# Kernel tuning notes

Measured on AMD Instinct MI355X. Metric: run time of the kernel, lower is better.

Reference implementation:

```python
import jax, jax.numpy as jnp
import numpy as np

E = 1024
H = 16
DH = E // H
S = 2048
K_NEIGHBOURS = 64
MASKING_VALUE = -1e10  # fp32 branch of the original module


def setup_inputs() -> dict:
    key = jax.random.key(0)
    ks = jax.random.split(key, 5)
    return {
        "x": jax.random.normal(ks[0], (S, E), dtype=jnp.float32),
        "W_qkv": jax.random.normal(ks[1], (3 * E, E), dtype=jnp.float32) * (E ** -0.5),
        "b_qkv": jax.random.normal(ks[2], (3 * E,), dtype=jnp.float32) * 0.02,
        "W_out": jax.random.normal(ks[3], (E, E), dtype=jnp.float32) * (E ** -0.5),
        "b_out": jax.random.normal(ks[4], (E,), dtype=jnp.float32) * 0.02,
    }


def _heads(t):
    # 's (h d) -> h s d'
    return t.reshape(S, H, DH).transpose(1, 0, 2)


def reference(x, W_qkv, b_qkv, W_out, b_out):
    scale = DH ** -0.5
    qkv = x @ W_qkv.T + b_qkv                      # [S, 3E]
    q, k, v = jnp.split(qkv, 3, axis=-1)
    q, k, v = _heads(q), _heads(k), _heads(v)      # [H, S, DH]
    scores = jnp.einsum('hsd,htd->hst', q, k) * scale  # [H, S, S]
    # banded mask: keep |i-j| <= K_NEIGHBOURS
    idx = jnp.arange(S)
    band = jnp.abs(idx[:, None] - idx[None, :]) <= K_NEIGHBOURS  # [S, S]
    scores = jnp.where(band[None, :, :], scores, MASKING_VALUE)
    attn = jax.nn.softmax(scores, axis=-1)
    out = jnp.einsum('hst,htd->hsd', attn, v)      # [H, S, DH]
    out = out.transpose(1, 0, 2).reshape(S, E)      # 'h s d -> s (h d)'
    out = out @ W_out.T + b_out
    return (out, scores)
```

## Files before the change

### kernel.cpp

```cpp
#include <hip/hip_runtime.h>

typedef unsigned short u16;
typedef __attribute__((ext_vector_type(8))) short short8;
typedef __attribute__((ext_vector_type(4))) short short4v;
typedef __attribute__((ext_vector_type(4))) float f32x4;

#define S_LEN 2048
#define EMB   1024
#define NH    16
#define NEGM  (-1e10f)

__device__ __forceinline__ u16 f2bf(float f) {
  unsigned u = __float_as_uint(f);
  u += 0x7fffu + ((u >> 16) & 1u);
  return (u16)(u >> 16);
}

__device__ __forceinline__ void async16(const u16* g, u16* l) {
  __builtin_amdgcn_global_load_lds(
      (const __attribute__((address_space(1))) unsigned int*)g,
      (__attribute__((address_space(3))) unsigned int*)l, 16, 0, 0);
}

__global__ __launch_bounds__(256) void cast3_kernel(
    const float* __restrict__ a, u16* __restrict__ oa, int na,
    const float* __restrict__ b, u16* __restrict__ ob, int nb,
    const float* __restrict__ c, u16* __restrict__ oc, int nc) {
  int t = (blockIdx.x * 256 + threadIdx.x) * 8;
  const float* in;
  u16* out;
  if (t < na) { in = a + t; out = oa + t; }
  else if (t < na + nb) { in = b + (t - na); out = ob + (t - na); }
  else if (t < na + nb + nc) { in = c + (t - na - nb); out = oc + (t - na - nb); }
  else return;
  f32x4 lo = *(const f32x4*)(in);
  f32x4 hi = *(const f32x4*)(in + 4);
  u16 r[8];
  r[0] = f2bf(lo.x); r[1] = f2bf(lo.y); r[2] = f2bf(lo.z); r[3] = f2bf(lo.w);
  r[4] = f2bf(hi.x); r[5] = f2bf(hi.y); r[6] = f2bf(hi.z); r[7] = f2bf(hi.w);
  *(short8*)(out) = *(short8*)r;
}

template <int BM, int BN, int OUT_BF16, int MINW>
__global__ __launch_bounds__(256, MINW) void gemm_kernel(
    const u16* __restrict__ A, const u16* __restrict__ B,
    const float* __restrict__ bias, void* __restrict__ Cout,
    int M, int N, int K, int grid_x, int gemm_blocks,
    float* __restrict__ fill_ptr, long long fill_f4, int fill_blocks) {
  __shared__ u16 As[BM * 64];
  __shared__ u16 Bs[BN * 64];
  const int b = blockIdx.x;
  const int tid = threadIdx.x;

  if (b >= gemm_blocks) {
    const long long fb = b - gemm_blocks;
    f32x4 neg = {NEGM, NEGM, NEGM, NEGM};
    f32x4* p = (f32x4*)fill_ptr;
    const long long stride = (long long)fill_blocks * 256;
    for (long long idx = fb * 256 + tid; idx < fill_f4; idx += stride)
      __builtin_nontemporal_store(neg, p + idx);
    return;
  }

  const int lane = tid & 63, wave = tid >> 6;
  const int lr = lane & 15, lg = lane >> 4;
  const int bx = b % grid_x, by = b / grid_x;
  const int m0 = by * BM, n0 = bx * BN;
  const int wm = (wave >> 1) * (BM / 2), wn = (wave & 1) * (BN / 2);
  constexpr int MI = BM / 32, NJ = BN / 32;

  f32x4 acc[MI][NJ];
#pragma unroll
  for (int i = 0; i < MI; ++i)
#pragma unroll
    for (int j = 0; j < NJ; ++j) acc[i][j] = (f32x4){0.f, 0.f, 0.f, 0.f};

  for (int kt = 0; kt < K; kt += 64) {
#pragma unroll
    for (int it = 0; it < BM / 32; ++it) {
      int f = it * 256 + tid;
      int row = f >> 3, ch = f & 7;
      int sch = ch ^ (row & 7);
      async16(A + (size_t)(m0 + row) * K + kt + sch * 8,
              &As[(it * 256 + wave * 64) * 8]);
    }
#pragma unroll
    for (int it = 0; it < BN / 32; ++it) {
      int f = it * 256 + tid;
      int row = f >> 3, ch = f & 7;
      int sch = ch ^ (row & 7);
      async16(B + (size_t)(n0 + row) * K + kt + sch * 8,
              &Bs[(it * 256 + wave * 64) * 8]);
    }
    __syncthreads();
#pragma unroll
    for (int kk = 0; kk < 2; ++kk) {
      short8 af[MI], bfr[NJ];
      int ca = kk * 4 + lg;
#pragma unroll
      for (int t = 0; t < MI; ++t) {
        int ra = wm + t * 16 + lr;
        af[t] = *(const short8*)&As[ra * 64 + ((ca ^ (ra & 7)) << 3)];
      }
#pragma unroll
      for (int t = 0; t < NJ; ++t) {
        int rb = wn + t * 16 + lr;
        bfr[t] = *(const short8*)&Bs[rb * 64 + ((ca ^ (rb & 7)) << 3)];
      }
#pragma unroll
      for (int i = 0; i < MI; ++i)
#pragma unroll
        for (int j = 0; j < NJ; ++j)
          acc[i][j] = __builtin_amdgcn_mfma_f32_16x16x32_bf16(af[i], bfr[j],
                                                              acc[i][j], 0, 0, 0);
    }
    __syncthreads();
  }
#pragma unroll
  for (int j = 0; j < NJ; ++j) {
    int col = n0 + wn + j * 16 + lr;
    float bv = bias[col];
#pragma unroll
    for (int i = 0; i < MI; ++i) {
#pragma unroll
      for (int r = 0; r < 4; ++r) {
        int row = m0 + wm + i * 16 + lg * 4 + r;
        float v = acc[i][j][r] + bv;
        if (OUT_BF16)
          ((u16*)Cout)[(size_t)row * N + col] = f2bf(v);
        else
          ((float*)Cout)[(size_t)row * N + col] = v;
      }
    }
  }
}

__global__ __launch_bounds__(256, 2) void attn_kernel(
    const u16* __restrict__ qkv,
    float* __restrict__ scores,
    u16* __restrict__ ctx) {
  const int h = blockIdx.y;
  const int i0 = blockIdx.x * 64;
  const int j0 = i0 - 64;
  const int tid = threadIdx.x;
  const int lane = tid & 63, wave = tid >> 6;
  const int lr = lane & 15, lg = lane >> 4;

  __shared__ u16 Kl[192 * 72];
  __shared__ u16 Vt[64 * 200];
  __shared__ u16 Pl[64 * 200];

#pragma unroll
  for (int it = 0; it < 6; ++it) {
    int f = it * 256 + tid;
    int jr = f >> 3, ch = f & 7;
    int j = j0 + jr;
    short8 kv = {0, 0, 0, 0, 0, 0, 0, 0};
    short8 vv = {0, 0, 0, 0, 0, 0, 0, 0};
    if ((unsigned)j < 2048u) {
      kv = *(const short8*)(qkv + (size_t)j * 3072 + 1024 + h * 64 + ch * 8);
      vv = *(const short8*)(qkv + (size_t)j * 3072 + 2048 + h * 64 + ch * 8);
    }
    *(short4v*)&Kl[jr * 72 + ch * 8] = __builtin_shufflevector(kv, kv, 0, 1, 2, 3);
    *(short4v*)&Kl[jr * 72 + ch * 8 + 4] = __builtin_shufflevector(kv, kv, 4, 5, 6, 7);
#pragma unroll
    for (int e = 0; e < 8; ++e) Vt[(ch * 8 + e) * 200 + jr] = (u16)(short)vv[e];
  }
  __syncthreads();

  short8 qf[2];
#pragma unroll
  for (int kk = 0; kk < 2; ++kk)
    qf[kk] = *(const short8*)(qkv + (size_t)(i0 + wave * 16 + lr) * 3072 +
                              h * 64 + kk * 32 + lg * 8);

  f32x4 sa[12];
#pragma unroll
  for (int n = 0; n < 12; ++n) sa[n] = (f32x4){0.f, 0.f, 0.f, 0.f};
#pragma unroll
  for (int kk = 0; kk < 2; ++kk) {
    short8 a = qf[kk];
#pragma unroll
    for (int nt = 0; nt < 12; ++nt) {
      int jr = nt * 16 + lr;
      int d = kk * 32 + lg * 8;
      short4v lo = *(const short4v*)&Kl[jr * 72 + d];
      short4v hi = *(const short4v*)&Kl[jr * 72 + d + 4];
      short8 b = __builtin_shufflevector(lo, hi, 0, 1, 2, 3, 4, 5, 6, 7);
      sa[nt] = __builtin_amdgcn_mfma_f32_16x16x32_bf16(a, b, sa[nt], 0, 0, 0);
    }
  }

  const float scale = 0.125f;
#pragma unroll
  for (int nt = 0; nt < 12; ++nt) {
    int j = j0 + nt * 16 + lr;
#pragma unroll
    for (int r = 0; r < 4; ++r) {
      int i = i0 + wave * 16 + lg * 4 + r;
      bool inb = (j >= i - 64) && (j <= i + 64);
      sa[nt][r] = inb ? sa[nt][r] * scale : NEGM;
    }
  }

  float* srow_base = scores + (size_t)h * 2048 * 2048;
#pragma unroll
  for (int r = 0; r < 4; ++r) {
    int i = i0 + wave * 16 + lg * 4 + r;
    float* rowp = srow_base + (size_t)i * 2048;
#pragma unroll
    for (int nt = 0; nt < 12; ++nt) {
      int j = j0 + nt * 16 + lr;
      if ((unsigned)j < 2048u) rowp[j] = sa[nt][r];
    }
  }

#pragma unroll
  for (int r = 0; r < 4; ++r) {
    float m = sa[0][r];
#pragma unroll
    for (int nt = 1; nt < 12; ++nt) m = fmaxf(m, sa[nt][r]);
#pragma unroll
    for (int off = 1; off < 16; off <<= 1) m = fmaxf(m, __shfl_xor(m, off));
    float p[12], s = 0.f;
#pragma unroll
    for (int nt = 0; nt < 12; ++nt) {
      p[nt] = __expf(sa[nt][r] - m);
      s += p[nt];
    }
#pragma unroll
    for (int off = 1; off < 16; off <<= 1) s += __shfl_xor(s, off);
    float inv = 1.f / s;
    int row = wave * 16 + lg * 4 + r;
#pragma unroll
    for (int nt = 0; nt < 12; ++nt)
      Pl[row * 200 + nt * 16 + lr] = f2bf(p[nt] * inv);
  }
  __syncthreads();

  f32x4 ca[4];
#pragma unroll
  for (int d = 0; d < 4; ++d) ca[d] = (f32x4){0.f, 0.f, 0.f, 0.f};
#pragma unroll
  for (int kk = 0; kk < 6; ++kk) {
    short8 a = *(const short8*)&Pl[(wave * 16 + lr) * 200 + kk * 32 + lg * 8];
#pragma unroll
    for (int dt = 0; dt < 4; ++dt) {
      short8 b = *(const short8*)&Vt[(dt * 16 + lr) * 200 + kk * 32 + lg * 8];
      ca[dt] = __builtin_amdgcn_mfma_f32_16x16x32_bf16(a, b, ca[dt], 0, 0, 0);
    }
  }
#pragma unroll
  for (int dt = 0; dt < 4; ++dt)
#pragma unroll
    for (int r = 0; r < 4; ++r) {
      int i = i0 + wave * 16 + lg * 4 + r;
      int d = h * 64 + dt * 16 + lr;
      ctx[(size_t)i * 1024 + d] = f2bf(ca[dt][r]);
    }
}

extern "C" void kernel_launch(void* const* d_in, const int* in_sizes, int n_in,
                              void* d_out, int out_size, void* d_ws, size_t ws_size,
                              hipStream_t stream) {
  const float* x    = (const float*)d_in[0];
  const float* Wqkv = (const float*)d_in[1];
  const float* bqkv = (const float*)d_in[2];
  const float* Wout = (const float*)d_in[3];
  const float* bout = (const float*)d_in[4];

  float* out    = (float*)d_out;
  float* scores = out + (size_t)S_LEN * EMB;

  char* ws = (char*)d_ws;
  u16* x_bf    = (u16*)(ws);
  u16* wqkv_bf = (u16*)(ws + (4u << 20));
  u16* wout_bf = (u16*)(ws + (10u << 20));
  u16* qkv_bf  = (u16*)(ws + (12u << 20));
  u16* ctx_bf  = (u16*)(ws + (24u << 20));

  const int n1 = S_LEN * EMB;
  const int n2 = 3 * EMB * EMB;
  const int n3 = EMB * EMB;

  cast3_kernel<<<(n1 + n2 + n3) / 8 / 256, 256, 0, stream>>>(
      x, x_bf, n1, Wqkv, wqkv_bf, n2, Wout, wout_bf, n3);

  const long long fill_f4 = (long long)NH * S_LEN * S_LEN / 4;
  gemm_kernel<128, 128, 1, 3><<<768, 256, 0, stream>>>(
      x_bf, wqkv_bf, bqkv, qkv_bf, S_LEN, 3 * EMB, EMB,
      3 * EMB / 128, 384,
      scores, fill_f4, 384);

  attn_kernel<<<dim3(S_LEN / 64, NH), 256, 0, stream>>>(qkv_bf, scores, ctx_bf);

  gemm_kernel<64, 128, 0, 2><<<256, 256, 0, stream>>>(
      ctx_bf, wout_bf, bout, out, S_LEN, EMB, EMB,
      EMB / 128, 256,
      nullptr, 0, 0);
}
```

Baseline: 332.1 us.

## Move masked-score fill from QKV GEMM blocks into attention kernel

The -1e10 fill of the full 16x2048x2048 score tensor used to run in extra blocks launched alongside the QKV projection GEMM, overwriting the whole tensor. The attention kernel now writes the masking value only to the columns outside its own 192-wide band window for each row tile, so band entries are no longer written twice. This cuts redundant stores but moves the large fill into the attention kernel, where it can no longer overlap with GEMM compute. It also lowers the QKV GEMM occupancy hint from 3 to 2 waves.

```diff
diff --git a/kernel.cpp b/kernel.cpp
--- a/kernel.cpp
+++ b/kernel.cpp
@@ -41,27 +41,15 @@
   *(short8*)(out) = *(short8*)r;
 }
 
-template <int BM, int BN, int OUT_BF16, int MINW>
-__global__ __launch_bounds__(256, MINW) void gemm_kernel(
+template <int BM, int BN, int OUT_BF16>
+__global__ __launch_bounds__(256, 2) void gemm_kernel(
     const u16* __restrict__ A, const u16* __restrict__ B,
     const float* __restrict__ bias, void* __restrict__ Cout,
-    int M, int N, int K, int grid_x, int gemm_blocks,
-    float* __restrict__ fill_ptr, long long fill_f4, int fill_blocks) {
+    int M, int N, int K, int grid_x) {
   __shared__ u16 As[BM * 64];
   __shared__ u16 Bs[BN * 64];
   const int b = blockIdx.x;
   const int tid = threadIdx.x;
-
-  if (b >= gemm_blocks) {
-    const long long fb = b - gemm_blocks;
-    f32x4 neg = {NEGM, NEGM, NEGM, NEGM};
-    f32x4* p = (f32x4*)fill_ptr;
-    const long long stride = (long long)fill_blocks * 256;
-    for (long long idx = fb * 256 + tid; idx < fill_f4; idx += stride)
-      __builtin_nontemporal_store(neg, p + idx);
-    return;
-  }
-
   const int lane = tid & 63, wave = tid >> 6;
   const int lr = lane & 15, lg = lane >> 4;
   const int bx = b % grid_x, by = b / grid_x;
@@ -258,6 +246,22 @@
       int d = h * 64 + dt * 16 + lr;
       ctx[(size_t)i * 1024 + d] = f2bf(ca[dt][r]);
     }
+
+  {
+    const int lw = (j0 > 0) ? j0 : 0;
+    const int rw = (j0 + 192 < 2048) ? (j0 + 192) : 2048;
+    const int nl = lw >> 2;
+    const int nr = (2048 - rw) >> 2;
+    const f32x4 neg = {NEGM, NEGM, NEGM, NEGM};
+    for (int r = 0; r < 64; ++r) {
+      f32x4* rowp = (f32x4*)(srow_base + (size_t)(i0 + r) * 2048);
+      for (int c = tid; c < nl; c += 256)
+        __builtin_nontemporal_store(neg, rowp + c);
+      f32x4* rowr = rowp + (rw >> 2);
+      for (int c = tid; c < nr; c += 256)
+        __builtin_nontemporal_store(neg, rowr + c);
+    }
+  }
 }
 
 extern "C" void kernel_launch(void* const* d_in, const int* in_sizes, int n_in,
@@ -286,16 +290,13 @@
   cast3_kernel<<<(n1 + n2 + n3) / 8 / 256, 256, 0, stream>>>(
       x, x_bf, n1, Wqkv, wqkv_bf, n2, Wout, wout_bf, n3);
 
-  const long long fill_f4 = (long long)NH * S_LEN * S_LEN / 4;
-  gemm_kernel<128, 128, 1, 3><<<768, 256, 0, stream>>>(
+  gemm_kernel<128, 128, 1><<<dim3(384), 256, 0, stream>>>(
       x_bf, wqkv_bf, bqkv, qkv_bf, S_LEN, 3 * EMB, EMB,
-      3 * EMB / 128, 384,
-      scores, fill_f4, 384);
+      3 * EMB / 128);
 
   attn_kernel<<<dim3(S_LEN / 64, NH), 256, 0, stream>>>(qkv_bf, scores, ctx_bf);
 
-  gemm_kernel<64, 128, 0, 2><<<256, 256, 0, stream>>>(
+  gemm_kernel<64, 128, 0><<<dim3(256), 256, 0, stream>>>(
       ctx_bf, wout_bf, bout, out, S_LEN, EMB, EMB,
-      EMB / 128, 256,
-      nullptr, 0, 0);
-}
+      EMB / 128);
+}
```

After: 351.7 us. +5.9%, slower.

## Split masked-scores fill across QKV and output GEMMs, skipping band window

Applied to the files above, without the earlier changes.

The -1e10 fill of the scores tensor was done entirely by extra blocks in the QKV projection GEMM. Now that GEMM fills only the first RSPLIT rows. The output-projection GEMM fills the remaining rows, writing only the columns outside the 192-wide window that the attention kernel already covers. The output-projection GEMM also moves to 64x64 tiles with more blocks and a higher occupancy hint. This spreads the bandwidth-heavy fill over two kernels so it overlaps more GEMM work and skips some redundant stores. It relies on the attention kernel writing exactly that window for the later rows.

```diff
diff --git a/kernel.cpp b/kernel.cpp
--- a/kernel.cpp
+++ b/kernel.cpp
@@ -9,6 +9,8 @@
 #define EMB   1024
 #define NH    16
 #define NEGM  (-1e10f)
+#define NROWS (NH * S_LEN)
+#define RSPLIT 20480
 
 __device__ __forceinline__ u16 f2bf(float f) {
   unsigned u = __float_as_uint(f);
@@ -46,19 +48,36 @@
     const u16* __restrict__ A, const u16* __restrict__ B,
     const float* __restrict__ bias, void* __restrict__ Cout,
     int M, int N, int K, int grid_x, int gemm_blocks,
-    float* __restrict__ fill_ptr, long long fill_f4, int fill_blocks) {
+    float* __restrict__ fill_ptr, long long fill_f4, int fill_blocks,
+    int fill_mode) {
   __shared__ u16 As[BM * 64];
   __shared__ u16 Bs[BN * 64];
   const int b = blockIdx.x;
   const int tid = threadIdx.x;
 
   if (b >= gemm_blocks) {
-    const long long fb = b - gemm_blocks;
-    f32x4 neg = {NEGM, NEGM, NEGM, NEGM};
-    f32x4* p = (f32x4*)fill_ptr;
-    const long long stride = (long long)fill_blocks * 256;
-    for (long long idx = fb * 256 + tid; idx < fill_f4; idx += stride)
-      __builtin_nontemporal_store(neg, p + idx);
+    const int fb = b - gemm_blocks;
+    const f32x4 neg = {NEGM, NEGM, NEGM, NEGM};
+    if (fill_mode == 0) {
+      f32x4* p = (f32x4*)fill_ptr;
+      const long long stride = (long long)fill_blocks * 256;
+      for (long long idx = (long long)fb * 256 + tid; idx < fill_f4; idx += stride)
+        __builtin_nontemporal_store(neg, p + idx);
+    } else {
+      for (int R = (int)fill_f4 + fb; R < NROWS; R += fill_blocks) {
+        int i  = R & (S_LEN - 1);
+        int i0 = i & ~63;
+        int lw = (i0 - 64 > 0) ? i0 - 64 : 0;
+        int rw = (i0 + 128 < S_LEN) ? i0 + 128 : S_LEN;
+        f32x4* rowp = (f32x4*)(fill_ptr + (size_t)R * S_LEN);
+        const int nl = lw >> 2, nr = (S_LEN - rw) >> 2;
+        for (int c = tid; c < nl; c += 256)
+          __builtin_nontemporal_store(neg, rowp + c);
+        f32x4* rowr = rowp + (rw >> 2);
+        for (int c = tid; c < nr; c += 256)
+          __builtin_nontemporal_store(neg, rowr + c);
+      }
+    }
     return;
   }
 
@@ -286,16 +305,17 @@
   cast3_kernel<<<(n1 + n2 + n3) / 8 / 256, 256, 0, stream>>>(
       x, x_bf, n1, Wqkv, wqkv_bf, n2, Wout, wout_bf, n3);
 
-  const long long fill_f4 = (long long)NH * S_LEN * S_LEN / 4;
   gemm_kernel<128, 128, 1, 3><<<768, 256, 0, stream>>>(
       x_bf, wqkv_bf, bqkv, qkv_bf, S_LEN, 3 * EMB, EMB,
       3 * EMB / 128, 384,
-      scores, fill_f4, 384);
+      scores, (long long)RSPLIT * (S_LEN / 4), 384,
+      0);
 
   attn_kernel<<<dim3(S_LEN / 64, NH), 256, 0, stream>>>(qkv_bf, scores, ctx_bf);
 
-  gemm_kernel<64, 128, 0, 2><<<256, 256, 0, stream>>>(
+  gemm_kernel<64, 64, 0, 3><<<768, 256, 0, stream>>>(
       ctx_bf, wout_bf, bout, out, S_LEN, EMB, EMB,
-      EMB / 128, 256,
-      nullptr, 0, 0);
-}
+      EMB / 64, 512,
+      scores, (long long)RSPLIT, 256,
+      1);
+}
```

Result: faster. 324.4 us (-2.3%).
